# Kernel tuning notes

Hardware: AMD Instinct MI355X
Metric: run time of the kernel (lower is better)

The kernel has to match this reference:

```python
import jax, jax.numpy as jnp
import numpy as np

B, L, K = 8, 512, 30
H, NUM_IN, NPTS = 128, 384, 8
EPS = 1e-8


def _linear_params(key, din, dout):
    kw, kb = jax.random.split(key)
    W = jax.random.normal(kw, (din, dout), jnp.float32) * 0.02
    b = jax.random.normal(kb, (dout,), jnp.float32) * 0.02
    return W, b


def setup_inputs() -> dict:
    key = jax.random.key(0)
    ks = jax.random.split(key, 10)
    h_V = jax.random.normal(ks[0], (B, L, H), jnp.float32)
    h_E = jax.random.normal(ks[1], (B, L, K, NUM_IN), jnp.float32)
    E_idx = jax.random.randint(ks[2], (B, L, K), 0, L)
    X_neighbors = jax.random.normal(ks[3], (B, L, K, 3, 3), jnp.float32) * 3.0
    mask_V = jnp.ones((B, L), jnp.float32)
    mask_attend = jnp.ones((B, L, K), jnp.float32)
    Wp, bp = _linear_params(ks[4], H, NPTS * 3)
    W1, b1 = _linear_params(ks[5], H + NUM_IN + 9 * NPTS, H)
    W2, b2 = _linear_params(ks[6], H, H)
    W3, b3 = _linear_params(ks[7], H, H)
    Wi, bi = _linear_params(ks[8], H, 4 * H)
    Wo, bo = _linear_params(ks[9], 4 * H, H)
    g1 = jnp.ones((H,), jnp.float32); be1 = jnp.zeros((H,), jnp.float32)
    g2 = jnp.ones((H,), jnp.float32); be2 = jnp.zeros((H,), jnp.float32)
    return dict(h_V=h_V, h_E=h_E, E_idx=E_idx, X_neighbors=X_neighbors,
                mask_V=mask_V, mask_attend=mask_attend,
                Wp=Wp, bp=bp, W1=W1, b1=b1, W2=W2, b2=b2, W3=W3, b3=b3,
                Wi=Wi, bi=bi, Wo=Wo, bo=bo, g1=g1, be1=be1, g2=g2, be2=be2)


def _frames(N, CA, C):
    # openfold Rigid.from_3_points (Gram-Schmidt): x-axis along CA-N, C in xy-plane
    e0 = CA - N
    e0 = e0 / jnp.sqrt(jnp.sum(e0 * e0, -1, keepdims=True) + EPS)
    e1 = C - CA
    e1 = e1 - e0 * jnp.sum(e0 * e1, -1, keepdims=True)
    e1 = e1 / jnp.sqrt(jnp.sum(e1 * e1, -1, keepdims=True) + EPS)
    e2 = jnp.cross(e0, e1)
    R = jnp.stack([e0, e1, e2], axis=-1)  # basis vectors as columns
    return R, CA


def _ln(x, g, b):
    m = jnp.mean(x, -1, keepdims=True)
    v = jnp.var(x, -1, keepdims=True)
    return (x - m) / jnp.sqrt(v + 1e-5) * g + b


def _forward(h_V, h_E, X_neighbors, mask_V, mask_attend, Wp, bp, W1, b1, W2, b2,
             W3, b3, Wi, bi, Wo, bo, g1, be1, g2, be2):
    gelu = lambda x: jax.nn.gelu(x, approximate=False)
    # per-neighbor backbone frames: [B,L,K,3,3], [B,L,K,3]
    R, t = _frames(X_neighbors[..., 0, :], X_neighbors[..., 1, :], X_neighbors[..., 2, :])
    h_V_prev = h_E[..., -H:]
    sh = h_E.shape[:-1]  # (B,L,K)
    p_ln = (h_V_prev @ Wp + bp).reshape(*sh, NPTS, 3)  # local points of each neighbor
    p_local = p_ln[:, :, 0]                            # [B,L,n,3] (self is neighbor 0)
    npg = jnp.einsum('blkij,blknj->blkni', R, p_ln) + t[..., None, :]  # global points
    p_global = npg[:, :, 0]
    pge = jnp.broadcast_to(p_global[:, :, None], npg.shape)
    ple = jnp.broadcast_to(p_local[:, :, None], npg.shape)
    pln = jnp.sqrt(jnp.sum(ple * ple, -1) + EPS)
    R0 = R[:, :, 0]; t0 = t[:, :, 0]  # self frame
    npl = jnp.einsum('blji,blknj->blkni', R0, npg - t0[:, :, None, None, :])  # invert_apply
    npl_norm = jnp.sqrt(jnp.sum(npl * npl, -1) + EPS)
    npg_norm = jnp.sqrt(jnp.sum((pge - npg) ** 2, -1) + EPS)
    node_expand = jnp.broadcast_to(h_V[:, :, None, :], (*sh, H))
    msg = jnp.concatenate([node_expand, h_E,
                           ple.reshape(*sh, -1), pln,
                           npl.reshape(*sh, -1), npl_norm, npg_norm], axis=-1)
    node_m = gelu(msg @ W1 + b1)
    node_m = gelu(node_m @ W2 + b2)
    node_m = node_m @ W3 + b3
    node_m = mask_attend[..., None] * node_m
    node_m = jnp.mean(node_m, axis=-2)
    h = _ln(h_V + node_m, g1, be1)  # dropout is identity in eval
    d = gelu(h @ Wi + bi) @ Wo + bo
    h = _ln(h + d, g2, be2)
    return mask_V[..., None] * h


def reference(h_V, h_E, E_idx, X_neighbors, mask_V, mask_attend, Wp, bp, W1, b1,
              W2, b2, W3, b3, Wi, bi, Wo, bo, g1, be1, g2, be2):
    # E_idx only defines the neighbor axis shape; geometry comes pre-gathered in X_neighbors/h_E
    return _forward(h_V, h_E, X_neighbors, mask_V, mask_attend, Wp, bp, W1, b1,
                    W2, b2, W3, b3, Wi, bi, Wo, bo, g1, be1, g2, be2)
```

## Files before the change

kernel.cpp:

```cpp
#include <hip/hip_runtime.h>

#define B_ 8
#define L_ 512
#define K_ 30
#define NIN_ 384
#define HES 11520
#define BUFW 136
#define GFW 96
#define PWU 4608
#define R0_OFF 0
#define T0_OFF 9
#define PL0_OFF 12
#define NPG_OFF 40
#define PLF_OFF 760
#define NM_OFF 640
#define GEOF_OFF 1520

#define W1F_OFF 0
#define W2F_OFF 77824
#define W3F_OFF 94208
#define WIF_OFF 110592
#define WOF_OFF 176128
#define WPF_OFF 241664

typedef __attribute__((ext_vector_type(8))) short short8;
typedef __attribute__((ext_vector_type(8))) unsigned short ushort8;
typedef __attribute__((ext_vector_type(4))) float floatx4;
typedef __attribute__((ext_vector_type(4))) float f32x4;

__device__ __forceinline__ float b2f(unsigned short u) {
    union { unsigned int i; float f; } x; x.i = ((unsigned int)u) << 16; return x.f;
}
__device__ __forceinline__ unsigned short f2b(float f) {
    unsigned int u = __builtin_bit_cast(unsigned int, f);
    return (unsigned short)((u + 0x7fffu + ((u >> 16) & 1u)) >> 16);
}
__device__ __forceinline__ float gelu_f(float x) {
    return 0.5f * x * (1.0f + erff(x * 0.70710678118654752440f));
}
__device__ __forceinline__ short8 pack8(const float* p) {
    f32x4 lo = *(const f32x4*)p;
    f32x4 hi = *(const f32x4*)(p + 4);
    short8 r;
    r[0] = (short)f2b(lo[0]); r[1] = (short)f2b(lo[1]);
    r[2] = (short)f2b(lo[2]); r[3] = (short)f2b(lo[3]);
    r[4] = (short)f2b(hi[0]); r[5] = (short)f2b(hi[1]);
    r[6] = (short)f2b(hi[2]); r[7] = (short)f2b(hi[3]);
    return r;
}
__device__ __forceinline__ float dot8(const float* hp, ushort8 v) {
    return hp[0] * b2f(v[0]) + hp[1] * b2f(v[1]) + hp[2] * b2f(v[2]) + hp[3] * b2f(v[3]) +
           hp[4] * b2f(v[4]) + hp[5] * b2f(v[5]) + hp[6] * b2f(v[6]) + hp[7] * b2f(v[7]);
}

__global__ __launch_bounds__(256) void prep_kernel(
        const float* __restrict__ W1, const float* __restrict__ W2,
        const float* __restrict__ W3, const float* __restrict__ Wi,
        const float* __restrict__ Wo, const float* __restrict__ Wp,
        unsigned short* __restrict__ ws) {
    int idx = blockIdx.x * 256 + threadIdx.x;
    if (idx < 94208 || (idx >= 241664 && idx < 245760)) {
        const float* in; int i, KC, Kreal, Nreal, Nld;
        if (idx < 77824)      { in = W1; i = idx;          KC = 19; Kreal = 584; Nreal = 128; Nld = 128; }
        else if (idx < 94208) { in = W2; i = idx - 77824;  KC = 4;  Kreal = 128; Nreal = 128; Nld = 128; }
        else                  { in = Wp; i = idx - 241664; KC = 4;  Kreal = 128; Nreal = 24;  Nld = 24;  }
        int f = i >> 9, r = i & 511;
        int ct = f / KC, kc = f % KC;
        int lane = r >> 3, j = r & 7;
        int q = lane >> 4, l = lane & 15;
        int k = kc * 32 + q * 8 + j, n = ct * 16 + l;
        ws[idx] = (k < Kreal && n < Nreal) ? f2b(in[k * Nld + n]) : (unsigned short)0;
    } else if (idx < 110592) {
        int i = idx - 94208;
        int f = i >> 9, r = i & 511;
        int ct = f >> 2, kc = f & 3;
        int lane = r >> 3, j = r & 7;
        int q = lane >> 4, l = lane & 15;
        ws[idx] = f2b(W3[(kc * 32 + q * 8 + j) * 128 + ct * 16 + l]);
    } else if (idx < 176128) {
        int i = idx - 110592;
        int c8 = i >> 12, r = i & 4095;
        int o = r >> 3, ii = r & 7;
        ws[idx] = f2b(Wi[(c8 * 8 + ii) * 512 + o]);
    } else if (idx < 241664) {
        int i = idx - 176128;
        int o8 = i >> 10, r = i & 1023;
        int c = r >> 3, ii = r & 7;
        ws[idx] = f2b(Wo[(o8 * 8 + ii) * 128 + c]);
    }
}

__global__ __launch_bounds__(128, 3) void main_kernel(
    const float* __restrict__ h_V,
    const float* __restrict__ h_E,
    const float* __restrict__ Xn,
    const float* __restrict__ mask_V,
    const float* __restrict__ mask_attend,
    const float* __restrict__ bp,
    const float* __restrict__ b1g,
    const float* __restrict__ b2g,
    const float* __restrict__ b3g,
    const float* __restrict__ big,
    const float* __restrict__ bog,
    const float* __restrict__ g1,
    const float* __restrict__ be1,
    const float* __restrict__ g2,
    const float* __restrict__ be2,
    const unsigned short* __restrict__ wsT,
    float* __restrict__ out) {

    __shared__ __align__(16) unsigned short lds[2 * PWU];

    const int tid  = threadIdx.x;
    const int wv   = tid >> 6;
    const int lane = tid & 63;
    const int quad = lane >> 4;
    const int l16  = lane & 15;
    const int ko   = quad * 8;
    const int site = blockIdx.x * 2 + wv;

    unsigned short* wl   = lds + wv * PWU;
    unsigned short* buf1 = wl;
    unsigned short* geoF = wl + GEOF_OFF;
    float*          Fv   = (float*)wl;

    const unsigned short* W1F = wsT + W1F_OFF;
    const unsigned short* W2F = wsT + W2F_OFF;
    const unsigned short* W3F = wsT + W3F_OFF;
    const unsigned short* WiF = wsT + WIF_OFF;
    const unsigned short* WoF = wsT + WOF_OFF;
    const unsigned short* WpF = wsT + WPF_OFF;

    const float* hEb = h_E + (size_t)site * HES;
    const float* hVb = h_V + site * 128;
    const short8 z8 = {0, 0, 0, 0, 0, 0, 0, 0};

    float maskR[2][4];
    for (int rt = 0; rt < 2; ++rt)
        for (int r = 0; r < 4; ++r) {
            int row = rt * 16 + quad * 4 + r;
            maskR[rt][r] = (row < K_) ? mask_attend[site * K_ + row] * (1.0f / 30.0f) : 0.0f;
        }

    float Rr[9], Tt[3];
    if (lane < K_) {
        const float* xp = Xn + ((size_t)site * K_ + lane) * 9;
        float Nx = xp[0], Ny = xp[1], Nz = xp[2];
        float Ax = xp[3], Ay = xp[4], Az = xp[5];
        float Cx = xp[6], Cy = xp[7], Cz = xp[8];
        float e0x = Ax - Nx, e0y = Ay - Ny, e0z = Az - Nz;
        float r0 = 1.0f / sqrtf(e0x * e0x + e0y * e0y + e0z * e0z + 1e-8f);
        e0x *= r0; e0y *= r0; e0z *= r0;
        float u1x = Cx - Ax, u1y = Cy - Ay, u1z = Cz - Az;
        float d = e0x * u1x + e0y * u1y + e0z * u1z;
        u1x -= e0x * d; u1y -= e0y * d; u1z -= e0z * d;
        float r1 = 1.0f / sqrtf(u1x * u1x + u1y * u1y + u1z * u1z + 1e-8f);
        u1x *= r1; u1y *= r1; u1z *= r1;
        Rr[0] = e0x; Rr[1] = u1x; Rr[2] = e0y * u1z - e0z * u1y;
        Rr[3] = e0y; Rr[4] = u1y; Rr[5] = e0z * u1x - e0x * u1z;
        Rr[6] = e0z; Rr[7] = u1z; Rr[8] = e0x * u1y - e0y * u1x;
        Tt[0] = Ax; Tt[1] = Ay; Tt[2] = Az;
    }

    {
        floatx4 a[2][2] = {{{0,0,0,0},{0,0,0,0}},{{0,0,0,0},{0,0,0,0}}};
        for (int kc = 0; kc < 4; ++kc) {
            int col = 256 + kc * 32 + ko;
            short8 fa0 = pack8(hEb + l16 * NIN_ + col);
            int r1 = 16 + l16;
            short8 fa1 = (r1 < K_) ? pack8(hEb + r1 * NIN_ + col) : z8;
            for (int ct = 0; ct < 2; ++ct) {
                short8 fb = *(const short8*)(WpF + (ct * 4 + kc) * 512 + lane * 8);
                a[0][ct] = __builtin_amdgcn_mfma_f32_16x16x32_bf16(fa0, fb, a[0][ct], 0, 0, 0);
                a[1][ct] = __builtin_amdgcn_mfma_f32_16x16x32_bf16(fa1, fb, a[1][ct], 0, 0, 0);
            }
        }
        for (int ct = 0; ct < 2; ++ct) {
            int ccol = ct * 16 + l16;
            if (ccol < 24) {
                float bpc = bp[ccol];
                for (int rt = 0; rt < 2; ++rt)
                    for (int i = 0; i < 4; ++i) {
                        int row = rt * 16 + quad * 4 + i;
                        if (row < K_) Fv[PLF_OFF + row * 24 + ccol] = a[rt][ct][i] + bpc;
                    }
            }
        }
    }

    if (lane < K_) {
        float pl[24];
        #pragma unroll
        for (int c = 0; c < 24; ++c) pl[c] = Fv[PLF_OFF + lane * 24 + c];
        if (lane == 0) {
            #pragma unroll
            for (int i = 0; i < 9; ++i) Fv[R0_OFF + i] = Rr[i];
            Fv[T0_OFF] = Tt[0]; Fv[T0_OFF + 1] = Tt[1]; Fv[T0_OFF + 2] = Tt[2];
            #pragma unroll
            for (int c = 0; c < 24; ++c) Fv[PL0_OFF + c] = pl[c];
        }
        #pragma unroll
        for (int n = 0; n < 8; ++n) {
            float p0 = pl[n * 3], p1 = pl[n * 3 + 1], p2 = pl[n * 3 + 2];
            #pragma unroll
            for (int i = 0; i < 3; ++i)
                Fv[NPG_OFF + lane * 24 + n * 3 + i] =
                    Rr[i * 3 + 0] * p0 + Rr[i * 3 + 1] * p1 + Rr[i * 3 + 2] * p2 + Tt[i];
        }
    }

    for (int id = lane; id < 720; id += 64) geoF[(id / 24) * GFW + 72 + id % 24] = 0;
    {
        float R00 = Fv[0], R01 = Fv[1], R02 = Fv[2], R03 = Fv[3], R04 = Fv[4];
        float R05 = Fv[5], R06 = Fv[6], R07 = Fv[7], R08 = Fv[8];
        float T00 = Fv[9], T01 = Fv[10], T02 = Fv[11];
        for (int id = lane; id < 240; id += 64) {
            int k = id >> 3, n = id & 7;
            float p0 = Fv[PL0_OFF + n * 3], p1 = Fv[PL0_OFF + n * 3 + 1], p2 = Fv[PL0_OFF + n * 3 + 2];
            float q0g = Fv[NPG_OFF + n * 3], q1g = Fv[NPG_OFF + n * 3 + 1], q2g = Fv[NPG_OFF + n * 3 + 2];
            float a0 = Fv[NPG_OFF + k * 24 + n * 3];
            float a1 = Fv[NPG_OFF + k * 24 + n * 3 + 1];
            float a2 = Fv[NPG_OFF + k * 24 + n * 3 + 2];
            float d0 = a0 - T00, d1 = a1 - T01, d2 = a2 - T02;
            float nl0 = R00 * d0 + R03 * d1 + R06 * d2;
            float nl1 = R01 * d0 + R04 * d1 + R07 * d2;
            float nl2 = R02 * d0 + R05 * d1 + R08 * d2;
            unsigned short* gf = geoF + k * GFW;
            gf[0 + n * 3] = f2b(p0); gf[1 + n * 3] = f2b(p1); gf[2 + n * 3] = f2b(p2);
            gf[24 + n] = f2b(sqrtf(p0 * p0 + p1 * p1 + p2 * p2 + 1e-8f));
            gf[32 + n * 3] = f2b(nl0); gf[33 + n * 3] = f2b(nl1); gf[34 + n * 3] = f2b(nl2);
            gf[56 + n] = f2b(sqrtf(nl0 * nl0 + nl1 * nl1 + nl2 * nl2 + 1e-8f));
            float q0 = q0g - a0, q1 = q1g - a1, q2 = q2g - a2;
            gf[64 + n] = f2b(sqrtf(q0 * q0 + q1 * q1 + q2 * q2 + 1e-8f));
        }
    }

    {
        floatx4 acc[2][8];
        for (int rt = 0; rt < 2; ++rt) for (int ct = 0; ct < 8; ++ct) acc[rt][ct] = (floatx4){0,0,0,0};
        for (int kc = 0; kc < 4; ++kc) {
            int col = kc * 32 + ko;
            short8 fa = pack8(hVb + col);
            for (int ct = 0; ct < 8; ++ct) {
                short8 fb = *(const short8*)(W1F + (ct * 19 + kc) * 512 + lane * 8);
                acc[0][ct] = __builtin_amdgcn_mfma_f32_16x16x32_bf16(fa, fb, acc[0][ct], 0, 0, 0);
                acc[1][ct] = __builtin_amdgcn_mfma_f32_16x16x32_bf16(fa, fb, acc[1][ct], 0, 0, 0);
            }
        }
        for (int kc = 0; kc < 12; ++kc) {
            int col = kc * 32 + ko;
            short8 fa0 = pack8(hEb + l16 * NIN_ + col);
            int r1 = 16 + l16;
            short8 fa1 = (r1 < K_) ? pack8(hEb + r1 * NIN_ + col) : z8;
            for (int ct = 0; ct < 8; ++ct) {
                short8 fb = *(const short8*)(W1F + (ct * 19 + 4 + kc) * 512 + lane * 8);
                acc[0][ct] = __builtin_amdgcn_mfma_f32_16x16x32_bf16(fa0, fb, acc[0][ct], 0, 0, 0);
                acc[1][ct] = __builtin_amdgcn_mfma_f32_16x16x32_bf16(fa1, fb, acc[1][ct], 0, 0, 0);
            }
        }
        for (int kc = 0; kc < 3; ++kc) {
            int col = kc * 32 + ko;
            short8 fa0 = *(const short8*)&geoF[l16 * GFW + col];
            int r1 = 16 + l16;
            short8 fa1 = (r1 < K_) ? *(const short8*)&geoF[r1 * GFW + col] : z8;
            for (int ct = 0; ct < 8; ++ct) {
                short8 fb = *(const short8*)(W1F + (ct * 19 + 16 + kc) * 512 + lane * 8);
                acc[0][ct] = __builtin_amdgcn_mfma_f32_16x16x32_bf16(fa0, fb, acc[0][ct], 0, 0, 0);
                acc[1][ct] = __builtin_amdgcn_mfma_f32_16x16x32_bf16(fa1, fb, acc[1][ct], 0, 0, 0);
            }
        }
        for (int ct = 0; ct < 8; ++ct) {
            int col = ct * 16 + l16;
            float bb = b1g[col];
            for (int rt = 0; rt < 2; ++rt)
                for (int r = 0; r < 4; ++r) {
                    int row = rt * 16 + quad * 4 + r;
                    buf1[row * BUFW + col] = f2b(gelu_f(acc[rt][ct][r] + bb));
                }
        }
    }

    {
        short8 Af[2][4];
        for (int kc = 0; kc < 4; ++kc) {
            Af[0][kc] = *(const short8*)&buf1[l16 * BUFW + kc * 32 + ko];
            Af[1][kc] = *(const short8*)&buf1[(16 + l16) * BUFW + kc * 32 + ko];
        }
        floatx4 acc[2][8];
        for (int rt = 0; rt < 2; ++rt) for (int ct = 0; ct < 8; ++ct) acc[rt][ct] = (floatx4){0,0,0,0};
        for (int kc = 0; kc < 4; ++kc)
            for (int ct = 0; ct < 8; ++ct) {
                short8 fb = *(const short8*)(W2F + (ct * 4 + kc) * 512 + lane * 8);
                acc[0][ct] = __builtin_amdgcn_mfma_f32_16x16x32_bf16(Af[0][kc], fb, acc[0][ct], 0, 0, 0);
                acc[1][ct] = __builtin_amdgcn_mfma_f32_16x16x32_bf16(Af[1][kc], fb, acc[1][ct], 0, 0, 0);
            }
        for (int ct = 0; ct < 8; ++ct) {
            int col = ct * 16 + l16;
            float bb = b2g[col];
            for (int rt = 0; rt < 2; ++rt)
                for (int r = 0; r < 4; ++r) {
                    int row = rt * 16 + quad * 4 + r;
                    buf1[row * BUFW + col] = f2b(gelu_f(acc[rt][ct][r] + bb));
                }
        }
    }

    {
        short8 Af[2][4];
        for (int kc = 0; kc < 4; ++kc) {
            Af[0][kc] = *(const short8*)&buf1[l16 * BUFW + kc * 32 + ko];
            Af[1][kc] = *(const short8*)&buf1[(16 + l16) * BUFW + kc * 32 + ko];
        }
        floatx4 acc[2][8];
        for (int rt = 0; rt < 2; ++rt) for (int ct = 0; ct < 8; ++ct) acc[rt][ct] = (floatx4){0,0,0,0};
        for (int kc = 0; kc < 4; ++kc)
            for (int ct = 0; ct < 8; ++ct) {
                short8 fb = *(const short8*)(W3F + (ct * 4 + kc) * 512 + lane * 8);
                acc[0][ct] = __builtin_amdgcn_mfma_f32_16x16x32_bf16(Af[0][kc], fb, acc[0][ct], 0, 0, 0);
                acc[1][ct] = __builtin_amdgcn_mfma_f32_16x16x32_bf16(Af[1][kc], fb, acc[1][ct], 0, 0, 0);
            }
        for (int ct = 0; ct < 8; ++ct) {
            int col = ct * 16 + l16;
            float bb = b3g[col];
            float cs = 0.0f;
            for (int rt = 0; rt < 2; ++rt)
                for (int r = 0; r < 4; ++r)
                    cs += (acc[rt][ct][r] + bb) * maskR[rt][r];
            cs += __shfl_xor(cs, 16, 64);
            cs += __shfl_xor(cs, 32, 64);
            if (lane < 16) Fv[NM_OFF + col] = cs;
        }
    }

    {
        int c0 = lane, c1 = lane + 64;
        float xb0 = hVb[c0] + Fv[NM_OFF + c0];
        float xb1 = hVb[c1] + Fv[NM_OFF + c1];
        float s = xb0 + xb1, q = xb0 * xb0 + xb1 * xb1;
        for (int o = 32; o; o >>= 1) { s += __shfl_xor(s, o, 64); q += __shfl_xor(q, o, 64); }
        float m = s * (1.0f / 128.0f);
        float inv = 1.0f / sqrtf(q * (1.0f / 128.0f) - m * m + 1e-5f);
        float h0 = (xb0 - m) * inv * g1[c0] + be1[c0];
        float h1 = (xb1 - m) * inv * g1[c1] + be1[c1];
        Fv[c0] = h0; Fv[c1] = h1;

        for (int j = 0; j < 8; ++j) {
            int o = lane + 64 * j;
            float sa = big[o], sb = 0.0f;
            for (int c8 = 0; c8 < 16; c8 += 2) {
                ushort8 v0 = *(const ushort8*)(WiF + c8 * 4096 + o * 8);
                ushort8 v1 = *(const ushort8*)(WiF + (c8 + 1) * 4096 + o * 8);
                sa += dot8(&Fv[c8 * 8], v0);
                sb += dot8(&Fv[c8 * 8 + 8], v1);
            }
            Fv[128 + o] = gelu_f(sa + sb);
        }

        float d0a = bog[c0], d0b = 0.0f, d1a = bog[c1], d1b = 0.0f;
        for (int o8 = 0; o8 < 64; o8 += 2) {
            ushort8 v0  = *(const ushort8*)(WoF + o8 * 1024 + c0 * 8);
            ushort8 v0n = *(const ushort8*)(WoF + (o8 + 1) * 1024 + c0 * 8);
            ushort8 v1  = *(const ushort8*)(WoF + o8 * 1024 + c1 * 8);
            ushort8 v1n = *(const ushort8*)(WoF + (o8 + 1) * 1024 + c1 * 8);
            const float* gp = &Fv[128 + o8 * 8];
            d0a += dot8(gp, v0);  d0b += dot8(gp + 8, v0n);
            d1a += dot8(gp, v1);  d1b += dot8(gp + 8, v1n);
        }
        float y0 = h0 + d0a + d0b, y1 = h1 + d1a + d1b;
        float s2 = y0 + y1, q2 = y0 * y0 + y1 * y1;
        for (int o = 32; o; o >>= 1) { s2 += __shfl_xor(s2, o, 64); q2 += __shfl_xor(q2, o, 64); }
        float m2 = s2 * (1.0f / 128.0f);
        float inv2 = 1.0f / sqrtf(q2 * (1.0f / 128.0f) - m2 * m2 + 1e-5f);
        float mv = mask_V[site];
        out[site * 128 + c0] = ((y0 - m2) * inv2 * g2[c0] + be2[c0]) * mv;
        out[site * 128 + c1] = ((y1 - m2) * inv2 * g2[c1] + be2[c1]) * mv;
    }
}

extern "C" void kernel_launch(void* const* d_in, const int* in_sizes, int n_in,
                              void* d_out, int out_size, void* d_ws, size_t ws_size,
                              hipStream_t stream) {
    const float* h_V = (const float*)d_in[0];
    const float* h_E = (const float*)d_in[1];
    const float* Xn  = (const float*)d_in[3];
    const float* mV  = (const float*)d_in[4];
    const float* mA  = (const float*)d_in[5];
    const float* Wp  = (const float*)d_in[6];
    const float* bp  = (const float*)d_in[7];
    const float* W1  = (const float*)d_in[8];
    const float* b1  = (const float*)d_in[9];
    const float* W2  = (const float*)d_in[10];
    const float* b2  = (const float*)d_in[11];
    const float* W3  = (const float*)d_in[12];
    const float* b3  = (const float*)d_in[13];
    const float* Wi  = (const float*)d_in[14];
    const float* bi  = (const float*)d_in[15];
    const float* Wo  = (const float*)d_in[16];
    const float* bo  = (const float*)d_in[17];
    const float* g1  = (const float*)d_in[18];
    const float* be1 = (const float*)d_in[19];
    const float* g2  = (const float*)d_in[20];
    const float* be2 = (const float*)d_in[21];
    unsigned short* ws = (unsigned short*)d_ws;
    float* out = (float*)d_out;

    prep_kernel<<<960, 256, 0, stream>>>(W1, W2, W3, Wi, Wo, Wp, ws);
    main_kernel<<<(B_ * L_) / 2, 128, 0, stream>>>(h_V, h_E, Xn, mV, mA, bp,
                                                   b1, b2, b3, bi, bo,
                                                   g1, be1, g2, be2, ws, out);
}
```

Before: 446.0 us.

## Split each site across two wavefronts, one per 16-row neighbor tile

Each block now handles one site instead of two, and the two wavefronts split the 30 neighbor rows into two 16-row MFMA tiles. The node-FFN and layernorm stages are spread over 128 threads, with block barriers and cross-wave partial sums passed through LDS. Per-thread register and LDS use drop, so launch bounds rise to allow more resident blocks and better latency hiding. The cost is twice as many blocks, each wave reading the weight fragments separately, and extra __syncthreads.

```diff
diff --git a/kernel.cpp b/kernel.cpp
--- a/kernel.cpp
+++ b/kernel.cpp
@@ -7,13 +7,16 @@
 #define HES 11520
 #define BUFW 136
 #define GFW 96
-#define PWU 4608
 #define R0_OFF 0
 #define T0_OFF 9
 #define PL0_OFF 12
 #define NPG_OFF 40
 #define PLF_OFF 760
-#define NM_OFF 640
+#define NM0_OFF 2200
+#define NM1_OFF 2328
+#define LNP_OFF 2456
+#define HARR_OFF 0
+#define GARR_OFF 128
 #define GEOF_OFF 1520
 
 #define W1F_OFF 0
@@ -90,7 +93,7 @@
     }
 }
 
-__global__ __launch_bounds__(128, 3) void main_kernel(
+__global__ __launch_bounds__(128, 6) void main_kernel(
     const float* __restrict__ h_V,
     const float* __restrict__ h_E,
     const float* __restrict__ Xn,
@@ -109,7 +112,7 @@
     const unsigned short* __restrict__ wsT,
     float* __restrict__ out) {
 
-    __shared__ __align__(16) unsigned short lds[2 * PWU];
+    __shared__ __align__(16) unsigned short lds[4928];
 
     const int tid  = threadIdx.x;
     const int wv   = tid >> 6;
@@ -117,12 +120,12 @@
     const int quad = lane >> 4;
     const int l16  = lane & 15;
     const int ko   = quad * 8;
-    const int site = blockIdx.x * 2 + wv;
-
-    unsigned short* wl   = lds + wv * PWU;
-    unsigned short* buf1 = wl;
-    unsigned short* geoF = wl + GEOF_OFF;
-    float*          Fv   = (float*)wl;
+    const int site = blockIdx.x;
+    const int rowB = wv * 16;
+
+    unsigned short* buf1 = lds;
+    unsigned short* geoF = lds + GEOF_OFF;
+    float*          Fv   = (float*)lds;
 
     const unsigned short* W1F = wsT + W1F_OFF;
     const unsigned short* W2F = wsT + W2F_OFF;
@@ -135,16 +138,17 @@
     const float* hVb = h_V + site * 128;
     const short8 z8 = {0, 0, 0, 0, 0, 0, 0, 0};
 
-    float maskR[2][4];
-    for (int rt = 0; rt < 2; ++rt)
-        for (int r = 0; r < 4; ++r) {
-            int row = rt * 16 + quad * 4 + r;
-            maskR[rt][r] = (row < K_) ? mask_attend[site * K_ + row] * (1.0f / 30.0f) : 0.0f;
-        }
-
+    float maskR[4];
+    for (int r = 0; r < 4; ++r) {
+        int row = rowB + quad * 4 + r;
+        maskR[r] = (row < K_) ? mask_attend[site * K_ + row] * (1.0f / 30.0f) : 0.0f;
+    }
+
+    const int kf = rowB + l16;
+    const bool fActive = (lane < 16) && (kf < K_);
     float Rr[9], Tt[3];
-    if (lane < K_) {
-        const float* xp = Xn + ((size_t)site * K_ + lane) * 9;
+    if (fActive) {
+        const float* xp = Xn + ((size_t)site * K_ + kf) * 9;
         float Nx = xp[0], Ny = xp[1], Nz = xp[2];
         float Ax = xp[3], Ay = xp[4], Az = xp[5];
         float Cx = xp[6], Cy = xp[7], Cz = xp[8];
@@ -163,36 +167,33 @@
     }
 
     {
-        floatx4 a[2][2] = {{{0,0,0,0},{0,0,0,0}},{{0,0,0,0},{0,0,0,0}}};
+        floatx4 a[2] = {{0,0,0,0},{0,0,0,0}};
         for (int kc = 0; kc < 4; ++kc) {
             int col = 256 + kc * 32 + ko;
-            short8 fa0 = pack8(hEb + l16 * NIN_ + col);
-            int r1 = 16 + l16;
-            short8 fa1 = (r1 < K_) ? pack8(hEb + r1 * NIN_ + col) : z8;
+            int r = rowB + l16;
+            short8 fa = (r < K_) ? pack8(hEb + r * NIN_ + col) : z8;
             for (int ct = 0; ct < 2; ++ct) {
                 short8 fb = *(const short8*)(WpF + (ct * 4 + kc) * 512 + lane * 8);
-                a[0][ct] = __builtin_amdgcn_mfma_f32_16x16x32_bf16(fa0, fb, a[0][ct], 0, 0, 0);
-                a[1][ct] = __builtin_amdgcn_mfma_f32_16x16x32_bf16(fa1, fb, a[1][ct], 0, 0, 0);
+                a[ct] = __builtin_amdgcn_mfma_f32_16x16x32_bf16(fa, fb, a[ct], 0, 0, 0);
             }
         }
         for (int ct = 0; ct < 2; ++ct) {
             int ccol = ct * 16 + l16;
             if (ccol < 24) {
                 float bpc = bp[ccol];
-                for (int rt = 0; rt < 2; ++rt)
-                    for (int i = 0; i < 4; ++i) {
-                        int row = rt * 16 + quad * 4 + i;
-                        if (row < K_) Fv[PLF_OFF + row * 24 + ccol] = a[rt][ct][i] + bpc;
-                    }
-            }
-        }
-    }
-
-    if (lane < K_) {
+                for (int i = 0; i < 4; ++i) {
+                    int row = rowB + quad * 4 + i;
+                    if (row < K_) Fv[PLF_OFF + row * 24 + ccol] = a[ct][i] + bpc;
+                }
+            }
+        }
+    }
+
+    if (fActive) {
         float pl[24];
         #pragma unroll
-        for (int c = 0; c < 24; ++c) pl[c] = Fv[PLF_OFF + lane * 24 + c];
-        if (lane == 0) {
+        for (int c = 0; c < 24; ++c) pl[c] = Fv[PLF_OFF + kf * 24 + c];
+        if (kf == 0) {
             #pragma unroll
             for (int i = 0; i < 9; ++i) Fv[R0_OFF + i] = Rr[i];
             Fv[T0_OFF] = Tt[0]; Fv[T0_OFF + 1] = Tt[1]; Fv[T0_OFF + 2] = Tt[2];
@@ -204,17 +205,18 @@
             float p0 = pl[n * 3], p1 = pl[n * 3 + 1], p2 = pl[n * 3 + 2];
             #pragma unroll
             for (int i = 0; i < 3; ++i)
-                Fv[NPG_OFF + lane * 24 + n * 3 + i] =
+                Fv[NPG_OFF + kf * 24 + n * 3 + i] =
                     Rr[i * 3 + 0] * p0 + Rr[i * 3 + 1] * p1 + Rr[i * 3 + 2] * p2 + Tt[i];
         }
     }
-
-    for (int id = lane; id < 720; id += 64) geoF[(id / 24) * GFW + 72 + id % 24] = 0;
+    __syncthreads();
+
+    for (int id = tid; id < 720; id += 128) geoF[(id / 24) * GFW + 72 + id % 24] = 0;
     {
         float R00 = Fv[0], R01 = Fv[1], R02 = Fv[2], R03 = Fv[3], R04 = Fv[4];
         float R05 = Fv[5], R06 = Fv[6], R07 = Fv[7], R08 = Fv[8];
         float T00 = Fv[9], T01 = Fv[10], T02 = Fv[11];
-        for (int id = lane; id < 240; id += 64) {
+        for (int id = tid; id < 240; id += 128) {
             int k = id >> 3, n = id & 7;
             float p0 = Fv[PL0_OFF + n * 3], p1 = Fv[PL0_OFF + n * 3 + 1], p2 = Fv[PL0_OFF + n * 3 + 2];
             float q0g = Fv[NPG_OFF + n * 3], q1g = Fv[NPG_OFF + n * 3 + 1], q2g = Fv[NPG_OFF + n * 3 + 2];
@@ -234,146 +236,141 @@
             gf[64 + n] = f2b(sqrtf(q0 * q0 + q1 * q1 + q2 * q2 + 1e-8f));
         }
     }
-
-    {
-        floatx4 acc[2][8];
-        for (int rt = 0; rt < 2; ++rt) for (int ct = 0; ct < 8; ++ct) acc[rt][ct] = (floatx4){0,0,0,0};
+    __syncthreads();
+
+    {
+        floatx4 acc[8];
+        for (int ct = 0; ct < 8; ++ct) acc[ct] = (floatx4){0,0,0,0};
         for (int kc = 0; kc < 4; ++kc) {
             int col = kc * 32 + ko;
             short8 fa = pack8(hVb + col);
             for (int ct = 0; ct < 8; ++ct) {
                 short8 fb = *(const short8*)(W1F + (ct * 19 + kc) * 512 + lane * 8);
-                acc[0][ct] = __builtin_amdgcn_mfma_f32_16x16x32_bf16(fa, fb, acc[0][ct], 0, 0, 0);
-                acc[1][ct] = __builtin_amdgcn_mfma_f32_16x16x32_bf16(fa, fb, acc[1][ct], 0, 0, 0);
+                acc[ct] = __builtin_amdgcn_mfma_f32_16x16x32_bf16(fa, fb, acc[ct], 0, 0, 0);
             }
         }
         for (int kc = 0; kc < 12; ++kc) {
             int col = kc * 32 + ko;
-            short8 fa0 = pack8(hEb + l16 * NIN_ + col);
-            int r1 = 16 + l16;
-            short8 fa1 = (r1 < K_) ? pack8(hEb + r1 * NIN_ + col) : z8;
+            int r = rowB + l16;
+            short8 fa = (r < K_) ? pack8(hEb + r * NIN_ + col) : z8;
             for (int ct = 0; ct < 8; ++ct) {
                 short8 fb = *(const short8*)(W1F + (ct * 19 + 4 + kc) * 512 + lane * 8);
-                acc[0][ct] = __builtin_amdgcn_mfma_f32_16x16x32_bf16(fa0, fb, acc[0][ct], 0, 0, 0);
-                acc[1][ct] = __builtin_amdgcn_mfma_f32_16x16x32_bf16(fa1, fb, acc[1][ct], 0, 0, 0);
+                acc[ct] = __builtin_amdgcn_mfma_f32_16x16x32_bf16(fa, fb, acc[ct], 0, 0, 0);
             }
         }
         for (int kc = 0; kc < 3; ++kc) {
             int col = kc * 32 + ko;
-            short8 fa0 = *(const short8*)&geoF[l16 * GFW + col];
-            int r1 = 16 + l16;
-            short8 fa1 = (r1 < K_) ? *(const short8*)&geoF[r1 * GFW + col] : z8;
+            int r = rowB + l16;
+            short8 fa = (r < K_) ? *(const short8*)&geoF[r * GFW + col] : z8;
             for (int ct = 0; ct < 8; ++ct) {
                 short8 fb = *(const short8*)(W1F + (ct * 19 + 16 + kc) * 512 + lane * 8);
-                acc[0][ct] = __builtin_amdgcn_mfma_f32_16x16x32_bf16(fa0, fb, acc[0][ct], 0, 0, 0);
-                acc[1][ct] = __builtin_amdgcn_mfma_f32_16x16x32_bf16(fa1, fb, acc[1][ct], 0, 0, 0);
-            }
-        }
+                acc[ct] = __builtin_amdgcn_mfma_f32_16x16x32_bf16(fa, fb, acc[ct], 0, 0, 0);
+            }
+        }
+        __syncthreads();
         for (int ct = 0; ct < 8; ++ct) {
             int col = ct * 16 + l16;
             float bb = b1g[col];
-            for (int rt = 0; rt < 2; ++rt)
-                for (int r = 0; r < 4; ++r) {
-                    int row = rt * 16 + quad * 4 + r;
-                    buf1[row * BUFW + col] = f2b(gelu_f(acc[rt][ct][r] + bb));
-                }
-        }
-    }
-
-    {
-        short8 Af[2][4];
-        for (int kc = 0; kc < 4; ++kc) {
-            Af[0][kc] = *(const short8*)&buf1[l16 * BUFW + kc * 32 + ko];
-            Af[1][kc] = *(const short8*)&buf1[(16 + l16) * BUFW + kc * 32 + ko];
-        }
-        floatx4 acc[2][8];
-        for (int rt = 0; rt < 2; ++rt) for (int ct = 0; ct < 8; ++ct) acc[rt][ct] = (floatx4){0,0,0,0};
+            for (int r = 0; r < 4; ++r) {
+                int row = rowB + quad * 4 + r;
+                buf1[row * BUFW + col] = f2b(gelu_f(acc[ct][r] + bb));
+            }
+        }
+    }
+
+    {
+        short8 Af[4];
+        for (int kc = 0; kc < 4; ++kc)
+            Af[kc] = *(const short8*)&buf1[(rowB + l16) * BUFW + kc * 32 + ko];
+        floatx4 acc[8];
+        for (int ct = 0; ct < 8; ++ct) acc[ct] = (floatx4){0,0,0,0};
         for (int kc = 0; kc < 4; ++kc)
             for (int ct = 0; ct < 8; ++ct) {
                 short8 fb = *(const short8*)(W2F + (ct * 4 + kc) * 512 + lane * 8);
-                acc[0][ct] = __builtin_amdgcn_mfma_f32_16x16x32_bf16(Af[0][kc], fb, acc[0][ct], 0, 0, 0);
-                acc[1][ct] = __builtin_amdgcn_mfma_f32_16x16x32_bf16(Af[1][kc], fb, acc[1][ct], 0, 0, 0);
+                acc[ct] = __builtin_amdgcn_mfma_f32_16x16x32_bf16(Af[kc], fb, acc[ct], 0, 0, 0);
             }
         for (int ct = 0; ct < 8; ++ct) {
             int col = ct * 16 + l16;
             float bb = b2g[col];
-            for (int rt = 0; rt < 2; ++rt)
-                for (int r = 0; r < 4; ++r) {
-                    int row = rt * 16 + quad * 4 + r;
-                    buf1[row * BUFW + col] = f2b(gelu_f(acc[rt][ct][r] + bb));
-                }
-        }
-    }
-
-    {
-        short8 Af[2][4];
-        for (int kc = 0; kc < 4; ++kc) {
-            Af[0][kc] = *(const short8*)&buf1[l16 * BUFW + kc * 32 + ko];
-            Af[1][kc] = *(const short8*)&buf1[(16 + l16) * BUFW + kc * 32 + ko];
-        }
-        floatx4 acc[2][8];
-        for (int rt = 0; rt < 2; ++rt) for (int ct = 0; ct < 8; ++ct) acc[rt][ct] = (floatx4){0,0,0,0};
+            for (int r = 0; r < 4; ++r) {
+                int row = rowB + quad * 4 + r;
+                buf1[row * BUFW + col] = f2b(gelu_f(acc[ct][r] + bb));
+            }
+        }
+    }
+
+    {
+        short8 Af[4];
+        for (int kc = 0; kc < 4; ++kc)
+            Af[kc] = *(const short8*)&buf1[(rowB + l16) * BUFW + kc * 32 + ko];
+        floatx4 acc[8];
+        for (int ct = 0; ct < 8; ++ct) acc[ct] = (floatx4){0,0,0,0};
         for (int kc = 0; kc < 4; ++kc)
             for (int ct = 0; ct < 8; ++ct) {
                 short8 fb = *(const short8*)(W3F + (ct * 4 + kc) * 512 + lane * 8);
-                acc[0][ct] = __builtin_amdgcn_mfma_f32_16x16x32_bf16(Af[0][kc], fb, acc[0][ct], 0, 0, 0);
-                acc[1][ct] = __builtin_amdgcn_mfma_f32_16x16x32_bf16(Af[1][kc], fb, acc[1][ct], 0, 0, 0);
-            }
+                acc[ct] = __builtin_amdgcn_mfma_f32_16x16x32_bf16(Af[kc], fb, acc[ct], 0, 0, 0);
+            }
+        const int nmo = wv ? NM1_OFF : NM0_OFF;
         for (int ct = 0; ct < 8; ++ct) {
             int col = ct * 16 + l16;
             float bb = b3g[col];
             float cs = 0.0f;
-            for (int rt = 0; rt < 2; ++rt)
-                for (int r = 0; r < 4; ++r)
-                    cs += (acc[rt][ct][r] + bb) * maskR[rt][r];
+            for (int r = 0; r < 4; ++r)
+                cs += (acc[ct][r] + bb) * maskR[r];
             cs += __shfl_xor(cs, 16, 64);
             cs += __shfl_xor(cs, 32, 64);
-            if (lane < 16) Fv[NM_OFF + col] = cs;
-        }
-    }
-
-    {
-        int c0 = lane, c1 = lane + 64;
-        float xb0 = hVb[c0] + Fv[NM_OFF + c0];
-        float xb1 = hVb[c1] + Fv[NM_OFF + c1];
-        float s = xb0 + xb1, q = xb0 * xb0 + xb1 * xb1;
+            if (lane < 16) Fv[nmo + col] = cs;
+        }
+    }
+    __syncthreads();
+
+    {
+        int c = tid;
+        float xb = hVb[c] + Fv[NM0_OFF + c] + Fv[NM1_OFF + c];
+        float s = xb, q = xb * xb;
         for (int o = 32; o; o >>= 1) { s += __shfl_xor(s, o, 64); q += __shfl_xor(q, o, 64); }
-        float m = s * (1.0f / 128.0f);
-        float inv = 1.0f / sqrtf(q * (1.0f / 128.0f) - m * m + 1e-5f);
-        float h0 = (xb0 - m) * inv * g1[c0] + be1[c0];
-        float h1 = (xb1 - m) * inv * g1[c1] + be1[c1];
-        Fv[c0] = h0; Fv[c1] = h1;
-
-        for (int j = 0; j < 8; ++j) {
-            int o = lane + 64 * j;
+        if (lane == 0) { Fv[LNP_OFF + wv * 2] = s; Fv[LNP_OFF + wv * 2 + 1] = q; }
+        __syncthreads();
+        float sT = Fv[LNP_OFF + 0] + Fv[LNP_OFF + 2];
+        float qT = Fv[LNP_OFF + 1] + Fv[LNP_OFF + 3];
+        float m = sT * (1.0f / 128.0f);
+        float inv = 1.0f / sqrtf(qT * (1.0f / 128.0f) - m * m + 1e-5f);
+        float h = (xb - m) * inv * g1[c] + be1[c];
+        Fv[HARR_OFF + c] = h;
+        __syncthreads();
+
+        for (int j = 0; j < 4; ++j) {
+            int o = tid + 128 * j;
             float sa = big[o], sb = 0.0f;
             for (int c8 = 0; c8 < 16; c8 += 2) {
                 ushort8 v0 = *(const ushort8*)(WiF + c8 * 4096 + o * 8);
                 ushort8 v1 = *(const ushort8*)(WiF + (c8 + 1) * 4096 + o * 8);
-                sa += dot8(&Fv[c8 * 8], v0);
-                sb += dot8(&Fv[c8 * 8 + 8], v1);
-            }
-            Fv[128 + o] = gelu_f(sa + sb);
-        }
-
-        float d0a = bog[c0], d0b = 0.0f, d1a = bog[c1], d1b = 0.0f;
+                sa += dot8(&Fv[HARR_OFF + c8 * 8], v0);
+                sb += dot8(&Fv[HARR_OFF + c8 * 8 + 8], v1);
+            }
+            Fv[GARR_OFF + o] = gelu_f(sa + sb);
+        }
+        __syncthreads();
+
+        float d0 = bog[c], d1 = 0.0f;
         for (int o8 = 0; o8 < 64; o8 += 2) {
-            ushort8 v0  = *(const ushort8*)(WoF + o8 * 1024 + c0 * 8);
-            ushort8 v0n = *(const ushort8*)(WoF + (o8 + 1) * 1024 + c0 * 8);
-            ushort8 v1  = *(const ushort8*)(WoF + o8 * 1024 + c1 * 8);
-            ushort8 v1n = *(const ushort8*)(WoF + (o8 + 1) * 1024 + c1 * 8);
-            const float* gp = &Fv[128 + o8 * 8];
-            d0a += dot8(gp, v0);  d0b += dot8(gp + 8, v0n);
-            d1a += dot8(gp, v1);  d1b += dot8(gp + 8, v1n);
-        }
-        float y0 = h0 + d0a + d0b, y1 = h1 + d1a + d1b;
-        float s2 = y0 + y1, q2 = y0 * y0 + y1 * y1;
+            ushort8 v0  = *(const ushort8*)(WoF + o8 * 1024 + c * 8);
+            ushort8 v0n = *(const ushort8*)(WoF + (o8 + 1) * 1024 + c * 8);
+            const float* gp = &Fv[GARR_OFF + o8 * 8];
+            d0 += dot8(gp, v0);
+            d1 += dot8(gp + 8, v0n);
+        }
+        float y = h + d0 + d1;
+        float s2 = y, q2 = y * y;
         for (int o = 32; o; o >>= 1) { s2 += __shfl_xor(s2, o, 64); q2 += __shfl_xor(q2, o, 64); }
-        float m2 = s2 * (1.0f / 128.0f);
-        float inv2 = 1.0f / sqrtf(q2 * (1.0f / 128.0f) - m2 * m2 + 1e-5f);
+        if (lane == 0) { Fv[LNP_OFF + 4 + wv * 2] = s2; Fv[LNP_OFF + 4 + wv * 2 + 1] = q2; }
+        __syncthreads();
+        float sT2 = Fv[LNP_OFF + 4] + Fv[LNP_OFF + 6];
+        float qT2 = Fv[LNP_OFF + 5] + Fv[LNP_OFF + 7];
+        float m2 = sT2 * (1.0f / 128.0f);
+        float inv2 = 1.0f / sqrtf(qT2 * (1.0f / 128.0f) - m2 * m2 + 1e-5f);
         float mv = mask_V[site];
-        out[site * 128 + c0] = ((y0 - m2) * inv2 * g2[c0] + be2[c0]) * mv;
-        out[site * 128 + c1] = ((y1 - m2) * inv2 * g2[c1] + be2[c1]) * mv;
+        out[site * 128 + c] = ((y - m2) * inv2 * g2[c] + be2[c]) * mv;
     }
 }
 
@@ -405,7 +402,7 @@
     float* out = (float*)d_out;
 
     prep_kernel<<<960, 256, 0, stream>>>(W1, W2, W3, Wi, Wo, Wp, ws);
-    main_kernel<<<(B_ * L_) / 2, 128, 0, stream>>>(h_V, h_E, Xn, mV, mA, bp,
-                                                   b1, b2, b3, bi, bo,
-                                                   g1, be1, g2, be2, ws, out);
-}
+    main_kernel<<<B_ * L_, 128, 0, stream>>>(h_V, h_E, Xn, mV, mA, bp,
+                                             b1, b2, b3, bi, bo,
+                                             g1, be1, g2, be2, ws, out);
+}
```

Measured after the change: 808.4 us. 81.3% more time.
